# Kernel tuning notes

Measured on AMD Instinct MI355X. Metric: run time of the kernel, lower is better.

The kernel has to match this reference:

```python
import jax, jax.numpy as jnp
import numpy as np

B, S, D, H, L, V = 2, 2048, 768, 12, 2, 32000
DH = D // H
DF = 4 * D
LN_EPS = 1e-5


def _pos_enc():
    # faithful to source: exponent uses 2*i/D with i already stepping by 2
    pos = jnp.arange(S, dtype=jnp.float32)[:, None]
    i = jnp.arange(0, D, 2, dtype=jnp.float32)
    ang = pos / (10000.0 ** (2.0 * i / D))
    enc = jnp.zeros((S, D), jnp.float32)
    enc = enc.at[:, 0::2].set(jnp.sin(ang)).at[:, 1::2].set(jnp.cos(ang))
    return enc


def _ln(x, g, b):
    m = jnp.mean(x, axis=-1, keepdims=True)
    v = jnp.mean((x - m) ** 2, axis=-1, keepdims=True)
    return (x - m) / jnp.sqrt(v + LN_EPS) * g + b


def _layer(x, p):
    Wq, bq, Wk, bk, Wv, bv, Wo, bo, g1, be1, W1, b1, W2, b2, g2, be2 = p
    q = (x @ Wq + bq).reshape(B, S, H, DH)
    k = (x @ Wk + bk).reshape(B, S, H, DH)
    v = (x @ Wv + bv).reshape(B, S, H, DH)
    # NOTE: source divides by sqrt(embed_dim), not sqrt(head_dim)
    attn = jnp.einsum('bqhd,bkhd->bhqk', q, k) / jnp.sqrt(jnp.float32(D))
    attn = jax.nn.softmax(attn, axis=-1)  # [B,H,S,S]
    o = jnp.einsum('bhqk,bkhd->bqhd', attn, v).reshape(B, S, D)
    o = o @ Wo + bo
    x = _ln(x + o, g1, be1)
    h = jax.nn.gelu(x @ W1 + b1, approximate=False)
    x = _ln(x + h @ W2 + b2, g2, be2)
    return x


def setup_inputs() -> dict:
    key = jax.random.key(0)
    ks = jax.random.split(key, 16)
    n = lambda k, shape: jax.random.normal(k, shape, dtype=jnp.float32) * 0.02
    return {
        'input_ids': jax.random.randint(ks[0], (B, S), 0, V),
        'embed_table': n(ks[1], (V, D)),
        'Wq': n(ks[2], (L, D, D)), 'bq': jnp.zeros((L, D), jnp.float32),
        'Wk': n(ks[3], (L, D, D)), 'bk': jnp.zeros((L, D), jnp.float32),
        'Wv': n(ks[4], (L, D, D)), 'bv': jnp.zeros((L, D), jnp.float32),
        'Wo': n(ks[5], (L, D, D)), 'bo': jnp.zeros((L, D), jnp.float32),
        'ln1_g': jnp.ones((L, D), jnp.float32), 'ln1_b': jnp.zeros((L, D), jnp.float32),
        'W1': n(ks[6], (L, D, DF)), 'b1': jnp.zeros((L, DF), jnp.float32),
        'W2': n(ks[7], (L, DF, D)), 'b2': jnp.zeros((L, D), jnp.float32),
        'ln2_g': jnp.ones((L, D), jnp.float32), 'ln2_b': jnp.zeros((L, D), jnp.float32),
        'Wd': n(ks[8], (D, D)), 'bd': jnp.zeros((D,), jnp.float32),
        'lnm_g': jnp.ones((D,), jnp.float32), 'lnm_b': jnp.zeros((D,), jnp.float32),
        'dec_b': jnp.zeros((V,), jnp.float32),
    }


def reference(input_ids, embed_table, Wq, bq, Wk, bk, Wv, bv, Wo, bo,
              ln1_g, ln1_b, W1, b1, W2, b2, ln2_g, ln2_b,
              Wd, bd, lnm_g, lnm_b, dec_b):
    x = embed_table[input_ids] + _pos_enc()[None]  # [B,S,D]

    def step(h, p):
        return _layer(h, p), None

    x, _ = jax.lax.scan(step, x, (Wq, bq, Wk, bk, Wv, bv, Wo, bo,
                                  ln1_g, ln1_b, W1, b1, W2, b2, ln2_g, ln2_b))
    # MLM head with decoder weight tied to embedding table
    h = jax.nn.gelu(x @ Wd + bd, approximate=False)
    h = _ln(h, lnm_g, lnm_b)
    return h @ embed_table.T + dec_b  # [B,S,V]
```

## Files before the change

kernel.cpp:

```cpp
#include <hip/hip_runtime.h>
#include <hip/hip_bf16.h>
#include <cstdint>

typedef __bf16 bf16x8 __attribute__((ext_vector_type(8)));
typedef float  f32x4  __attribute__((ext_vector_type(4)));
typedef unsigned short u16;
typedef u16 u16x8 __attribute__((ext_vector_type(8)));

__device__ __forceinline__ u16 f2bf(float f) {
    union { float f; uint32_t u; } x{f};
    uint32_t u = x.u;
    return (u16)((u + 0x7fffu + ((u >> 16) & 1u)) >> 16);
}

__device__ __forceinline__ float gelu_f(float x) {
    return 0.5f * x * (1.0f + erff(x * 0.70710678118654752f));
}

__device__ __forceinline__ void gl_lds16(const void* g, void* l) {
    __builtin_amdgcn_global_load_lds(
        (__attribute__((address_space(1))) void*)(void*)g,
        (__attribute__((address_space(3))) void*)l, 16, 0, 0);
}

#define MFMA16(a, b, c) __builtin_amdgcn_mfma_f32_16x16x32_bf16((a), (b), (c), 0, 0, 0)
#define SB0 __builtin_amdgcn_sched_barrier(0)

template<int EPI, int OUTF32, int LOC>
__global__ __launch_bounds__(256, 2) void gemm_bf16(
    const u16* __restrict__ A, const u16* __restrict__ Bt,
    const float* __restrict__ bias, void* __restrict__ Cout,
    int N_, int K_)
{
    __shared__ u16 lA[128 * 64];
    __shared__ u16 lB[128 * 64];
    const int tid  = threadIdx.x;
    const int lane = tid & 63;
    const int wave = tid >> 6;
    const int wr = wave >> 1, wc = wave & 1;
    long row0, col0;
    if (LOC) {
        const int bid = blockIdx.x;
        const int chunk = bid >> 9, rem = bid & 511;
        row0 = (long)(rem & 31) * 128;
        col0 = (long)(chunk * 16 + (rem >> 5)) * 128;
    } else {
        row0 = (long)blockIdx.y * 128;
        col0 = (long)blockIdx.x * 128;
    }

    f32x4 acc[4][4];
#pragma unroll
    for (int i = 0; i < 4; ++i)
#pragma unroll
        for (int j = 0; j < 4; ++j)
#pragma unroll
            for (int t = 0; t < 4; ++t) acc[i][j][t] = 0.f;

    int sRow[4], sKb[4];
#pragma unroll
    for (int t = 0; t < 4; ++t) {
        int byteoff = (wave * 4 + t) * 1024 + lane * 16;
        int r = byteoff >> 7;
        sRow[t] = r;
        sKb[t]  = (byteoff & 127) ^ ((r & 7) << 4);
    }
    const int laneRC = lane & 15;
    const int laneK2 = (lane >> 4) * 16;

    for (int k0 = 0; k0 < K_; k0 += 64) {
#pragma unroll
        for (int t = 0; t < 4; ++t) {
            const int cb = (wave * 4 + t) * 1024;
            gl_lds16(A  + (row0 + sRow[t]) * K_ + k0 + (sKb[t] >> 1), (char*)lA + cb);
            gl_lds16(Bt + (col0 + sRow[t]) * K_ + k0 + (sKb[t] >> 1), (char*)lB + cb);
        }
        __syncthreads();
#pragma unroll
        for (int kk = 0; kk < 2; ++kk) {
            bf16x8 af[4], bfr[4];
#pragma unroll
            for (int i = 0; i < 4; ++i) {
                int r = wr * 64 + i * 16 + laneRC;
                af[i] = *(const bf16x8*)((const char*)lA + r * 128 + ((kk * 64 + laneK2) ^ ((r & 7) << 4)));
            }
#pragma unroll
            for (int j = 0; j < 4; ++j) {
                int n = wc * 64 + j * 16 + laneRC;
                bfr[j] = *(const bf16x8*)((const char*)lB + n * 128 + ((kk * 64 + laneK2) ^ ((n & 7) << 4)));
            }
#pragma unroll
            for (int i = 0; i < 4; ++i)
#pragma unroll
                for (int j = 0; j < 4; ++j)
                    acc[i][j] = MFMA16(af[i], bfr[j], acc[i][j]);
        }
        __syncthreads();
    }

#pragma unroll
    for (int j = 0; j < 4; ++j) {
        const long cidx = col0 + wc * 64 + j * 16 + laneRC;
        const float bvv = bias[cidx];
#pragma unroll
        for (int i = 0; i < 4; ++i) {
            const long rbase = row0 + wr * 64 + i * 16 + ((lane >> 4) << 2);
#pragma unroll
            for (int t = 0; t < 4; ++t) {
                float v = acc[i][j][t] + bvv;
                if (EPI) v = gelu_f(v);
                const long off = (rbase + t) * N_ + cidx;
                if (OUTF32) ((float*)Cout)[off] = v;
                else        ((u16*)Cout)[off]  = f2bf(v);
            }
        }
    }
}

template<int EPI, int OUTF32>
__global__ __launch_bounds__(256, 4) void gemm64(
    const u16* __restrict__ A, const u16* __restrict__ Bt,
    const float* __restrict__ bias, void* __restrict__ Cout,
    int N_, int K_)
{
    __shared__ u16 lA[64 * 64];
    __shared__ u16 lB[64 * 64];
    const int tid  = threadIdx.x;
    const int lane = tid & 63;
    const int wave = tid >> 6;
    const int wr = wave >> 1, wc = wave & 1;
    const long row0 = (long)blockIdx.y * 64;
    const long col0 = (long)blockIdx.x * 64;

    f32x4 acc[2][2];
#pragma unroll
    for (int i = 0; i < 2; ++i)
#pragma unroll
        for (int j = 0; j < 2; ++j)
#pragma unroll
            for (int t = 0; t < 4; ++t) acc[i][j][t] = 0.f;

    int sRow[2], sKb[2];
#pragma unroll
    for (int t = 0; t < 2; ++t) {
        int byteoff = (wave * 2 + t) * 1024 + lane * 16;
        int r = byteoff >> 7;
        sRow[t] = r;
        sKb[t]  = (byteoff & 127) ^ ((r & 7) << 4);
    }
    const int laneRC = lane & 15;
    const int laneK2 = (lane >> 4) * 16;

    for (int k0 = 0; k0 < K_; k0 += 64) {
#pragma unroll
        for (int t = 0; t < 2; ++t) {
            const int cb = (wave * 2 + t) * 1024;
            gl_lds16(A  + (row0 + sRow[t]) * K_ + k0 + (sKb[t] >> 1), (char*)lA + cb);
            gl_lds16(Bt + (col0 + sRow[t]) * K_ + k0 + (sKb[t] >> 1), (char*)lB + cb);
        }
        __syncthreads();
#pragma unroll
        for (int kk = 0; kk < 2; ++kk) {
            bf16x8 af[2], bfr[2];
#pragma unroll
            for (int i = 0; i < 2; ++i) {
                int r = wr * 32 + i * 16 + laneRC;
                af[i] = *(const bf16x8*)((const char*)lA + r * 128 + ((kk * 64 + laneK2) ^ ((r & 7) << 4)));
            }
#pragma unroll
            for (int j = 0; j < 2; ++j) {
                int n = wc * 32 + j * 16 + laneRC;
                bfr[j] = *(const bf16x8*)((const char*)lB + n * 128 + ((kk * 64 + laneK2) ^ ((n & 7) << 4)));
            }
#pragma unroll
            for (int i = 0; i < 2; ++i)
#pragma unroll
                for (int j = 0; j < 2; ++j)
                    acc[i][j] = MFMA16(af[i], bfr[j], acc[i][j]);
        }
        __syncthreads();
    }

#pragma unroll
    for (int j = 0; j < 2; ++j) {
        const long cidx = col0 + wc * 32 + j * 16 + laneRC;
        const float bvv = bias[cidx];
#pragma unroll
        for (int i = 0; i < 2; ++i) {
            const long rbase = row0 + wr * 32 + i * 16 + ((lane >> 4) << 2);
#pragma unroll
            for (int t = 0; t < 4; ++t) {
                float v = acc[i][j][t] + bvv;
                if (EPI) v = gelu_f(v);
                const long off = (rbase + t) * N_ + cidx;
                if (OUTF32) ((float*)Cout)[off] = v;
                else        ((u16*)Cout)[off]  = f2bf(v);
            }
        }
    }
}

__global__ __launch_bounds__(256, 3) void attn_fwd(
    const u16* __restrict__ qkv, u16* __restrict__ outb, float scale)
{
    __shared__ u16 lQ[64 * 64];
    __shared__ u16 lK[2][64 * 64];
    __shared__ u16 lVt[2][64 * 64];
    __shared__ u16 lP[64 * 64];
    const int bh = blockIdx.x;
    const int b = bh / 12, h = bh % 12;
    const int q0 = blockIdx.y * 64;
    const int tid = threadIdx.x, lane = tid & 63, wave = tid >> 6;
    const long baseQ = (long)b * 2048 * 2304 + h * 64;
    const long baseK = baseQ + 768;
    const long baseV = baseQ + 1536;
    const int laneRC = lane & 15;
    const int laneK2 = (lane >> 4) * 16;

    int stR[2], stC[2];
#pragma unroll
    for (int t = 0; t < 2; ++t) {
        const int byteoff = (wave * 2 + t) * 1024 + lane * 16;
        const int r = byteoff >> 7;
        stR[t] = r;
        stC[t] = ((byteoff & 127) ^ ((r & 7) << 4)) >> 1;
    }

#define STAGEK(BUF, KB0) do {                                                    \
    _Pragma("unroll") for (int t = 0; t < 2; ++t)                                \
        gl_lds16(qkv + baseK + (long)((KB0) + stR[t]) * 2304 + stC[t],           \
                 (char*)lK[BUF] + (wave * 2 + t) * 1024);                        \
} while (0)

#pragma unroll
    for (int t = 0; t < 2; ++t)
        gl_lds16(qkv + baseQ + (long)(q0 + stR[t]) * 2304 + stC[t],
                 (char*)lQ + (wave * 2 + t) * 1024);
    STAGEK(0, 0);
    u16x8 vA0, vA1;
    {
        const u16x8* gv = (const u16x8*)(qkv + baseV + (long)lane * 2304 + wave * 16);
        vA0 = gv[0]; vA1 = gv[1];
    }
    __syncthreads();

    bf16x8 qf[2];
#pragma unroll
    for (int kk = 0; kk < 2; ++kk) {
        int r = wave * 16 + laneRC;
        qf[kk] = *(const bf16x8*)((const char*)lQ + r * 128 + ((kk * 64 + laneK2) ^ ((r & 7) << 4)));
    }

    bf16x8 onesf;
#pragma unroll
    for (int j = 0; j < 8; ++j) onesf[j] = (__bf16)1.0f;

    float mrun[4];
    f32x4 oacc[4], oaccS;
#pragma unroll
    for (int r = 0; r < 4; ++r) mrun[r] = -1e30f;
#pragma unroll
    for (int dc = 0; dc < 4; ++dc)
#pragma unroll
        for (int t = 0; t < 4; ++t) oacc[dc][t] = 0.f;
#pragma unroll
    for (int t = 0; t < 4; ++t) oaccS[t] = 0.f;

    u16x8 vB0 = vA0, vB1 = vA1;
    for (int kt = 0; kt < 32; ++kt) {
        const int cur = kt & 1;
        asm volatile("s_waitcnt vmcnt(0)" ::: "memory");
        SB0;
        {
            const int kv = lane, dg = wave;
            char* vt = (char*)lVt[cur];
#pragma unroll
            for (int j = 0; j < 8; ++j) {
                int d0 = dg * 16 + j;
                *(u16*)(vt + d0 * 128 + ((kv * 2) ^ ((d0 & 7) << 4))) = vA0[j];
                int d1 = dg * 16 + 8 + j;
                *(u16*)(vt + d1 * 128 + ((kv * 2) ^ ((d1 & 7) << 4))) = vA1[j];
            }
        }
        __builtin_amdgcn_s_barrier();
        SB0;
        if (kt + 1 < 32) {
            STAGEK(cur ^ 1, (kt + 1) * 64);
            const u16x8* gv = (const u16x8*)(qkv + baseV + (long)((kt + 1) * 64 + lane) * 2304 + wave * 16);
            vB0 = gv[0]; vB1 = gv[1];
        }
        const char* lKc = (const char*)lK[cur];
        const char* lVc = (const char*)lVt[cur];

        f32x4 s[4];
#pragma unroll
        for (int cb = 0; cb < 4; ++cb)
#pragma unroll
            for (int t = 0; t < 4; ++t) s[cb][t] = 0.f;
        __builtin_amdgcn_s_setprio(1);
#pragma unroll
        for (int kk = 0; kk < 2; ++kk) {
            bf16x8 kf[4];
#pragma unroll
            for (int cb = 0; cb < 4; ++cb) {
                int kr = cb * 16 + laneRC;
                kf[cb] = *(const bf16x8*)(lKc + kr * 128 + ((kk * 64 + laneK2) ^ ((kr & 7) << 4)));
            }
#pragma unroll
            for (int cb = 0; cb < 4; ++cb)
                s[cb] = MFMA16(qf[kk], kf[cb], s[cb]);
        }
        __builtin_amdgcn_s_setprio(0);

        {
            float tm[4];
#pragma unroll
            for (int r = 0; r < 4; ++r) {
                float v = fmaxf(fmaxf(s[0][r], s[1][r]), fmaxf(s[2][r], s[3][r])) * scale;
#pragma unroll
                for (int msk = 1; msk < 16; msk <<= 1) v = fmaxf(v, __shfl_xor(v, msk, 64));
                tm[r] = v;
            }
            float ex = fmaxf(fmaxf(tm[0] - mrun[0], tm[1] - mrun[1]),
                             fmaxf(tm[2] - mrun[2], tm[3] - mrun[3]));
            float mn[4];
            if (__ballot(ex > 8.0f)) {
                float corr[4];
#pragma unroll
                for (int r = 0; r < 4; ++r) {
                    mn[r] = fmaxf(mrun[r], tm[r]);
                    corr[r] = __expf(mrun[r] - mn[r]);
                    mrun[r] = mn[r];
                }
                const int srcl = ((lane & 15) >> 2) << 4;
                float c0 = __shfl(corr[0], srcl, 64);
                float c1 = __shfl(corr[1], srcl, 64);
                float c2 = __shfl(corr[2], srcl, 64);
                float c3 = __shfl(corr[3], srcl, 64);
                const int selr = (lane & 15) & 3;
                float cp = selr == 0 ? c0 : (selr == 1 ? c1 : (selr == 2 ? c2 : c3));
#pragma unroll
                for (int dc = 0; dc < 4; ++dc)
#pragma unroll
                    for (int t = 0; t < 4; ++t) oacc[dc][t] *= cp;
#pragma unroll
                for (int t = 0; t < 4; ++t) oaccS[t] *= cp;
            } else {
#pragma unroll
                for (int r = 0; r < 4; ++r) mn[r] = mrun[r];
            }
#pragma unroll
            for (int cb2 = 0; cb2 < 4; ++cb2) {
                int pcol = cb2 * 16 + laneRC;
#pragma unroll
                for (int r = 0; r < 4; ++r) {
                    float pv = __expf(s[cb2][r] * scale - mn[r]);
                    int prow = wave * 16 + ((lane >> 4) << 2) + r;
                    *(u16*)((char*)lP + prow * 128 + ((pcol * 2) ^ ((prow & 7) << 4))) = f2bf(pv);
                }
            }
        }

        __builtin_amdgcn_s_setprio(1);
#pragma unroll
        for (int kk = 0; kk < 2; ++kk) {
            bf16x8 pf, vf[4];
            {
                int pr = wave * 16 + laneRC;
                pf = *(const bf16x8*)((const char*)lP + pr * 128 + ((kk * 64 + laneK2) ^ ((pr & 7) << 4)));
            }
#pragma unroll
            for (int dc = 0; dc < 4; ++dc) {
                int d = dc * 16 + laneRC;
                vf[dc] = *(const bf16x8*)(lVc + d * 128 + ((kk * 64 + laneK2) ^ ((d & 7) << 4)));
            }
#pragma unroll
            for (int dc = 0; dc < 4; ++dc)
                oacc[dc] = MFMA16(vf[dc], pf, oacc[dc]);
            oaccS = MFMA16(onesf, pf, oaccS);
        }
        __builtin_amdgcn_s_setprio(0);
        vA0 = vB0; vA1 = vB1;
    }
#undef STAGEK

    const float inv = 1.0f / oaccS[0];
    const long rowq = (long)b * 2048 + q0 + wave * 16 + (lane & 15);
#pragma unroll
    for (int dc = 0; dc < 4; ++dc) {
        const int colb = h * 64 + dc * 16 + ((lane >> 4) << 2);
        ushort4 st;
        st.x = f2bf(oacc[dc][0] * inv);
        st.y = f2bf(oacc[dc][1] * inv);
        st.z = f2bf(oacc[dc][2] * inv);
        st.w = f2bf(oacc[dc][3] * inv);
        *(ushort4*)(outb + rowq * 768 + colb) = st;
    }
}

__global__ __launch_bounds__(256) void ln_fused(
    const float* __restrict__ a, const float* __restrict__ bres,
    const float* __restrict__ g, const float* __restrict__ be,
    float* __restrict__ outf, u16* __restrict__ outb)
{
    const int wave = threadIdx.x >> 6, lane = threadIdx.x & 63;
    const int row = blockIdx.x * 4 + wave;
    const size_t rbase = (size_t)row * 768;
    float4 v[3];
    float s1 = 0.f, s2 = 0.f;
#pragma unroll
    for (int i = 0; i < 3; ++i) {
        const int c = lane * 4 + i * 256;
        float4 x = *(const float4*)(a + rbase + c);
        if (bres) {
            const float4 y = *(const float4*)(bres + rbase + c);
            x.x += y.x; x.y += y.y; x.z += y.z; x.w += y.w;
        }
        v[i] = x;
        s1 += x.x + x.y + x.z + x.w;
        s2 += x.x * x.x + x.y * x.y + x.z * x.z + x.w * x.w;
    }
#pragma unroll
    for (int m = 1; m < 64; m <<= 1) { s1 += __shfl_xor(s1, m, 64); s2 += __shfl_xor(s2, m, 64); }
    const float mean = s1 * (1.f / 768.f);
    const float var  = s2 * (1.f / 768.f) - mean * mean;
    const float rstd = rsqrtf(var + 1e-5f);
#pragma unroll
    for (int i = 0; i < 3; ++i) {
        const int c = lane * 4 + i * 256;
        const float4 gg = *(const float4*)(g + c);
        const float4 bb = *(const float4*)(be + c);
        float4 y;
        y.x = (v[i].x - mean) * rstd * gg.x + bb.x;
        y.y = (v[i].y - mean) * rstd * gg.y + bb.y;
        y.z = (v[i].z - mean) * rstd * gg.z + bb.z;
        y.w = (v[i].w - mean) * rstd * gg.w + bb.w;
        if (outf) *(float4*)(outf + rbase + c) = y;
        ushort4 u; u.x = f2bf(y.x); u.y = f2bf(y.y); u.z = f2bf(y.z); u.w = f2bf(y.w);
        *(ushort4*)(outb + rbase + c) = u;
    }
}

struct TP9 { const float* s[9]; u16* d[9]; };
__global__ void transpose_multi(TP9 p, int R, int C)
{
    __shared__ float t[32][33];
    const float* in = p.s[blockIdx.z];
    u16* out = p.d[blockIdx.z];
    const int c0 = blockIdx.x * 32, r0 = blockIdx.y * 32;
    const int tx = threadIdx.x, ty = threadIdx.y;
#pragma unroll
    for (int i = 0; i < 4; ++i)
        t[ty + 8 * i][tx] = in[(size_t)(r0 + ty + 8 * i) * C + c0 + tx];
    __syncthreads();
#pragma unroll
    for (int i = 0; i < 4; ++i)
        out[(size_t)(c0 + ty + 8 * i) * R + r0 + tx] = f2bf(t[tx][ty + 8 * i]);
}

__global__ void cvt_bf16_k(const float* __restrict__ in, u16* __restrict__ out, long n)
{
    long i = ((long)blockIdx.x * 256 + threadIdx.x) * 4;
    if (i >= n) return;
    const float4 f = *(const float4*)(in + i);
    ushort4 u; u.x = f2bf(f.x); u.y = f2bf(f.y); u.z = f2bf(f.z); u.w = f2bf(f.w);
    *(ushort4*)(out + i) = u;
}

__global__ void concat_bias(const float* __restrict__ bq, const float* __restrict__ bk,
                            const float* __restrict__ bv, float* __restrict__ out, int total)
{
    int i = blockIdx.x * 256 + threadIdx.x;
    if (i >= total) return;
    int l = i / 2304, j = i - l * 2304;
    float v = (j < 768) ? bq[l * 768 + j]
            : (j < 1536) ? bk[l * 768 + j - 768]
            : bv[l * 768 + j - 1536];
    out[i] = v;
}

__global__ __launch_bounds__(256) void embed_pe(
    const int* __restrict__ ids, const float* __restrict__ table,
    float* __restrict__ xf, u16* __restrict__ xb)
{
    const int idx = blockIdx.x * 256 + threadIdx.x;
    const int row = idx / 768, d = idx - row * 768;
    const int s = row & 2047;
    const float e = table[(long)ids[row] * 768 + d];
    const int j = d >> 1;
    const float ang = (float)s * __expf(-0.011992630692677324f * (float)(4 * j));
    const float pe = (d & 1) ? __cosf(ang) : __sinf(ang);
    const float v = e + pe;
    xf[idx] = v;
    xb[idx] = f2bf(v);
}

extern "C" void kernel_launch(void* const* d_in, const int* in_sizes, int n_in,
                              void* d_out, int out_size, void* d_ws, size_t ws_size,
                              hipStream_t stream)
{
    const int S = 2048, D = 768, H = 12, L = 2, V = 32000, DF = 3072, M = 4096, NQKV = 2304;
    (void)in_sizes; (void)n_in; (void)out_size; (void)ws_size; (void)H; (void)S;

    const int*   ids  = (const int*)  d_in[0];
    const float* emb  = (const float*)d_in[1];
    const float* Wq   = (const float*)d_in[2];
    const float* bq   = (const float*)d_in[3];
    const float* Wk   = (const float*)d_in[4];
    const float* bk   = (const float*)d_in[5];
    const float* Wv   = (const float*)d_in[6];
    const float* bv   = (const float*)d_in[7];
    const float* Wo   = (const float*)d_in[8];
    const float* bo   = (const float*)d_in[9];
    const float* ln1g = (const float*)d_in[10];
    const float* ln1b = (const float*)d_in[11];
    const float* W1   = (const float*)d_in[12];
    const float* b1   = (const float*)d_in[13];
    const float* W2   = (const float*)d_in[14];
    const float* b2   = (const float*)d_in[15];
    const float* ln2g = (const float*)d_in[16];
    const float* ln2b = (const float*)d_in[17];
    const float* Wd   = (const float*)d_in[18];
    const float* bd   = (const float*)d_in[19];
    const float* lnmg = (const float*)d_in[20];
    const float* lnmb = (const float*)d_in[21];
    const float* decb = (const float*)d_in[22];

    char* p = (char*)d_ws;
    auto carve = [&](size_t bytes) { char* r = p; p += (bytes + 255) & ~(size_t)255; return r; };
    u16*   embB  = (u16*)  carve((size_t)V * D * 2);
    u16*   wqkvT = (u16*)  carve((size_t)L * NQKV * D * 2);
    float* bqkv  = (float*)carve((size_t)L * NQKV * 4);
    u16*   woT   = (u16*)  carve((size_t)L * D * D * 2);
    u16*   w1T   = (u16*)  carve((size_t)L * DF * D * 2);
    u16*   w2T   = (u16*)  carve((size_t)L * D * DF * 2);
    u16*   wdT   = (u16*)  carve((size_t)D * D * 2);
    float* xf    = (float*)carve((size_t)M * D * 4);
    u16*   xb    = (u16*)  carve((size_t)M * D * 2);
    u16*   qkvB  = (u16*)  carve((size_t)M * NQKV * 2);
    u16*   aoB   = (u16*)  carve((size_t)M * D * 2);
    float* tmpf  = (float*)carve((size_t)M * D * 4);
    u16*   hB    = (u16*)  carve((size_t)M * DF * 2);

    dim3 t32x8(32, 8);
    cvt_bf16_k<<<((long)V * D / 4 + 255) / 256, 256, 0, stream>>>(emb, embB, (long)V * D);
    {
        TP9 t9;
        for (int l = 0; l < L; ++l) {
            t9.s[l * 4 + 0] = Wq + (size_t)l * D * D; t9.d[l * 4 + 0] = wqkvT + (size_t)l * NQKV * D;
            t9.s[l * 4 + 1] = Wk + (size_t)l * D * D; t9.d[l * 4 + 1] = wqkvT + (size_t)l * NQKV * D + (size_t)D * D;
            t9.s[l * 4 + 2] = Wv + (size_t)l * D * D; t9.d[l * 4 + 2] = wqkvT + (size_t)l * NQKV * D + (size_t)2 * D * D;
            t9.s[l * 4 + 3] = Wo + (size_t)l * D * D; t9.d[l * 4 + 3] = woT + (size_t)l * D * D;
        }
        t9.s[8] = Wd; t9.d[8] = wdT;
        transpose_multi<<<dim3(24, 24, 9), t32x8, 0, stream>>>(t9, D, D);
        TP9 tw1; tw1.s[0] = W1; tw1.d[0] = w1T; tw1.s[1] = W1 + (size_t)D * DF; tw1.d[1] = w1T + (size_t)DF * D;
        transpose_multi<<<dim3(96, 24, 2), t32x8, 0, stream>>>(tw1, D, DF);
        TP9 tw2; tw2.s[0] = W2; tw2.d[0] = w2T; tw2.s[1] = W2 + (size_t)DF * D; tw2.d[1] = w2T + (size_t)D * DF;
        transpose_multi<<<dim3(24, 96, 2), t32x8, 0, stream>>>(tw2, DF, D);
    }
    concat_bias<<<(L * NQKV + 255) / 256, 256, 0, stream>>>(bq, bk, bv, bqkv, L * NQKV);
    embed_pe<<<M * D / 256, 256, 0, stream>>>(ids, emb, xf, xb);

    const float scale = 0.036084391824351615f;
    for (int l = 0; l < L; ++l) {
        gemm_bf16<0, 0, 0><<<dim3(NQKV / 128, M / 128), 256, 0, stream>>>(xb, wqkvT + (size_t)l * NQKV * D, bqkv + l * NQKV, qkvB, NQKV, D);
        attn_fwd<<<dim3(24, 32), 256, 0, stream>>>(qkvB, aoB, scale);
        gemm64<0, 1><<<dim3(D / 64, M / 64), 256, 0, stream>>>(aoB, woT + (size_t)l * D * D, bo + l * D, tmpf, D, D);
        ln_fused<<<M / 4, 256, 0, stream>>>(xf, tmpf, ln1g + l * D, ln1b + l * D, xf, xb);
        gemm_bf16<1, 0, 0><<<dim3(DF / 128, M / 128), 256, 0, stream>>>(xb, w1T + (size_t)l * DF * D, b1 + l * DF, hB, DF, D);
        gemm64<0, 1><<<dim3(D / 64, M / 64), 256, 0, stream>>>(hB, w2T + (size_t)l * D * DF, b2 + l * D, tmpf, D, DF);
        ln_fused<<<M / 4, 256, 0, stream>>>(xf, tmpf, ln2g + l * D, ln2b + l * D, xf, xb);
    }
    gemm64<1, 1><<<dim3(D / 64, M / 64), 256, 0, stream>>>(xb, wdT, bd, tmpf, D, D);
    ln_fused<<<M / 4, 256, 0, stream>>>(tmpf, nullptr, lnmg, lnmb, nullptr, aoB);
    gemm_bf16<0, 1, 1><<<V / 128 * 32, 256, 0, stream>>>(aoB, embB, decb, (float*)d_out, V, D);
}
```

Baseline: 763.8 us.

## Split-K FFN down-proj into LN, lazy softmax max updates, fuse prep kernels

The FFN down-projection now uses the 128-tile GEMM with 4-way split-K. Partial sums go to four fp32 buffers that the following LayerNorm adds up, with the bias applied only by the first split. This aims to raise occupancy for the narrow N=768 GEMM with long K. In attention, the running-max check and rescale now run only every fourth key tile, and the embedding conversion, embed+PE and bias concat are merged into one launch. Skipping max updates relies on exp not overflowing within the window, and split-K adds extra fp32 traffic.

```diff
diff --git a/kernel.cpp b/kernel.cpp
--- a/kernel.cpp
+++ b/kernel.cpp
@@ -26,7 +26,7 @@
 #define MFMA16(a, b, c) __builtin_amdgcn_mfma_f32_16x16x32_bf16((a), (b), (c), 0, 0, 0)
 #define SB0 __builtin_amdgcn_sched_barrier(0)
 
-template<int EPI, int OUTF32, int LOC>
+template<int EPI, int OUTF32, int LOC, int SPLITK>
 __global__ __launch_bounds__(256, 2) void gemm_bf16(
     const u16* __restrict__ A, const u16* __restrict__ Bt,
     const float* __restrict__ bias, void* __restrict__ Cout,
@@ -48,6 +48,8 @@
         row0 = (long)blockIdx.y * 128;
         col0 = (long)blockIdx.x * 128;
     }
+    const int KS = K_ / SPLITK;
+    const int kz = (SPLITK > 1) ? blockIdx.z * KS : 0;
 
     f32x4 acc[4][4];
 #pragma unroll
@@ -68,7 +70,7 @@
     const int laneRC = lane & 15;
     const int laneK2 = (lane >> 4) * 16;
 
-    for (int k0 = 0; k0 < K_; k0 += 64) {
+    for (int k0 = kz; k0 < kz + KS; k0 += 64) {
 #pragma unroll
         for (int t = 0; t < 4; ++t) {
             const int cb = (wave * 4 + t) * 1024;
@@ -98,10 +100,11 @@
         __syncthreads();
     }
 
+    float* outF = (float*)Cout + (SPLITK > 1 ? (long)blockIdx.z * 4096 * N_ : 0);
 #pragma unroll
     for (int j = 0; j < 4; ++j) {
         const long cidx = col0 + wc * 64 + j * 16 + laneRC;
-        const float bvv = bias[cidx];
+        const float bvv = (SPLITK == 1 || blockIdx.z == 0) ? bias[cidx] : 0.f;
 #pragma unroll
         for (int i = 0; i < 4; ++i) {
             const long rbase = row0 + wr * 64 + i * 16 + ((lane >> 4) << 2);
@@ -110,8 +113,8 @@
                 float v = acc[i][j][t] + bvv;
                 if (EPI) v = gelu_f(v);
                 const long off = (rbase + t) * N_ + cidx;
-                if (OUTF32) ((float*)Cout)[off] = v;
-                else        ((u16*)Cout)[off]  = f2bf(v);
+                if (OUTF32) outF[off] = v;
+                else        ((u16*)Cout)[off] = f2bf(v);
             }
         }
     }
@@ -312,7 +315,7 @@
         }
         __builtin_amdgcn_s_setprio(0);
 
-        {
+        if ((kt & 3) == 0) {
             float tm[4];
 #pragma unroll
             for (int r = 0; r < 4; ++r) {
@@ -323,14 +326,13 @@
             }
             float ex = fmaxf(fmaxf(tm[0] - mrun[0], tm[1] - mrun[1]),
                              fmaxf(tm[2] - mrun[2], tm[3] - mrun[3]));
-            float mn[4];
             if (__ballot(ex > 8.0f)) {
                 float corr[4];
 #pragma unroll
                 for (int r = 0; r < 4; ++r) {
-                    mn[r] = fmaxf(mrun[r], tm[r]);
-                    corr[r] = __expf(mrun[r] - mn[r]);
-                    mrun[r] = mn[r];
+                    float mnew = fmaxf(mrun[r], tm[r]);
+                    corr[r] = __expf(mrun[r] - mnew);
+                    mrun[r] = mnew;
                 }
                 const int srcl = ((lane & 15) >> 2) << 4;
                 float c0 = __shfl(corr[0], srcl, 64);
@@ -345,19 +347,16 @@
                     for (int t = 0; t < 4; ++t) oacc[dc][t] *= cp;
 #pragma unroll
                 for (int t = 0; t < 4; ++t) oaccS[t] *= cp;
-            } else {
-#pragma unroll
-                for (int r = 0; r < 4; ++r) mn[r] = mrun[r];
-            }
-#pragma unroll
-            for (int cb2 = 0; cb2 < 4; ++cb2) {
-                int pcol = cb2 * 16 + laneRC;
-#pragma unroll
-                for (int r = 0; r < 4; ++r) {
-                    float pv = __expf(s[cb2][r] * scale - mn[r]);
-                    int prow = wave * 16 + ((lane >> 4) << 2) + r;
-                    *(u16*)((char*)lP + prow * 128 + ((pcol * 2) ^ ((prow & 7) << 4))) = f2bf(pv);
-                }
+            }
+        }
+#pragma unroll
+        for (int cb2 = 0; cb2 < 4; ++cb2) {
+            int pcol = cb2 * 16 + laneRC;
+#pragma unroll
+            for (int r = 0; r < 4; ++r) {
+                float pv = __expf(s[cb2][r] * scale - mrun[r]);
+                int prow = wave * 16 + ((lane >> 4) << 2) + r;
+                *(u16*)((char*)lP + prow * 128 + ((pcol * 2) ^ ((prow & 7) << 4))) = f2bf(pv);
             }
         }
 
@@ -398,8 +397,9 @@
     }
 }
 
+template<int NP>
 __global__ __launch_bounds__(256) void ln_fused(
-    const float* __restrict__ a, const float* __restrict__ bres,
+    const float* __restrict__ a, const float* __restrict__ parts, long pstride,
     const float* __restrict__ g, const float* __restrict__ be,
     float* __restrict__ outf, u16* __restrict__ outb)
 {
@@ -412,8 +412,9 @@
     for (int i = 0; i < 3; ++i) {
         const int c = lane * 4 + i * 256;
         float4 x = *(const float4*)(a + rbase + c);
-        if (bres) {
-            const float4 y = *(const float4*)(bres + rbase + c);
+#pragma unroll
+        for (int p = 0; p < NP; ++p) {
+            const float4 y = *(const float4*)(parts + (size_t)p * pstride + rbase + c);
             x.x += y.x; x.y += y.y; x.z += y.z; x.w += y.w;
         }
         v[i] = x;
@@ -458,41 +459,41 @@
         out[(size_t)(c0 + ty + 8 * i) * R + r0 + tx] = f2bf(t[tx][ty + 8 * i]);
 }
 
-__global__ void cvt_bf16_k(const float* __restrict__ in, u16* __restrict__ out, long n)
-{
-    long i = ((long)blockIdx.x * 256 + threadIdx.x) * 4;
-    if (i >= n) return;
-    const float4 f = *(const float4*)(in + i);
-    ushort4 u; u.x = f2bf(f.x); u.y = f2bf(f.y); u.z = f2bf(f.z); u.w = f2bf(f.w);
-    *(ushort4*)(out + i) = u;
-}
-
-__global__ void concat_bias(const float* __restrict__ bq, const float* __restrict__ bk,
-                            const float* __restrict__ bv, float* __restrict__ out, int total)
-{
-    int i = blockIdx.x * 256 + threadIdx.x;
-    if (i >= total) return;
-    int l = i / 2304, j = i - l * 2304;
-    float v = (j < 768) ? bq[l * 768 + j]
-            : (j < 1536) ? bk[l * 768 + j - 768]
-            : bv[l * 768 + j - 1536];
-    out[i] = v;
-}
-
-__global__ __launch_bounds__(256) void embed_pe(
-    const int* __restrict__ ids, const float* __restrict__ table,
-    float* __restrict__ xf, u16* __restrict__ xb)
-{
-    const int idx = blockIdx.x * 256 + threadIdx.x;
-    const int row = idx / 768, d = idx - row * 768;
-    const int s = row & 2047;
-    const float e = table[(long)ids[row] * 768 + d];
-    const int j = d >> 1;
-    const float ang = (float)s * __expf(-0.011992630692677324f * (float)(4 * j));
-    const float pe = (d & 1) ? __cosf(ang) : __sinf(ang);
-    const float v = e + pe;
-    xf[idx] = v;
-    xb[idx] = f2bf(v);
+__global__ __launch_bounds__(256) void prep_misc(
+    const float* __restrict__ emb, u16* __restrict__ embB,
+    const int* __restrict__ ids, float* __restrict__ xf, u16* __restrict__ xb,
+    const float* __restrict__ bq, const float* __restrict__ bk,
+    const float* __restrict__ bv, float* __restrict__ bqkv)
+{
+    const long A = 6144000;
+    const long B = 3145728;
+    long t = (long)blockIdx.x * 256 + threadIdx.x;
+    if (t < A) {
+        const long i = t * 4;
+        const float4 f = *(const float4*)(emb + i);
+        ushort4 u; u.x = f2bf(f.x); u.y = f2bf(f.y); u.z = f2bf(f.z); u.w = f2bf(f.w);
+        *(ushort4*)(embB + i) = u;
+    } else if (t < A + B) {
+        const int idx = (int)(t - A);
+        const int row = idx / 768, d = idx - row * 768;
+        const int s = row & 2047;
+        const float e = emb[(long)ids[row] * 768 + d];
+        const int j = d >> 1;
+        const float ang = (float)s * __expf(-0.011992630692677324f * (float)(4 * j));
+        const float pe = (d & 1) ? __cosf(ang) : __sinf(ang);
+        const float v = e + pe;
+        xf[idx] = v;
+        xb[idx] = f2bf(v);
+    } else {
+        const int i = (int)(t - A - B);
+        if (i < 4608) {
+            int l = i / 2304, j = i - l * 2304;
+            float v = (j < 768) ? bq[l * 768 + j]
+                    : (j < 1536) ? bk[l * 768 + j - 768]
+                    : bv[l * 768 + j - 1536];
+            bqkv[i] = v;
+        }
+    }
 }
 
 extern "C" void kernel_launch(void* const* d_in, const int* in_sizes, int n_in,
@@ -539,11 +540,12 @@
     u16*   xb    = (u16*)  carve((size_t)M * D * 2);
     u16*   qkvB  = (u16*)  carve((size_t)M * NQKV * 2);
     u16*   aoB   = (u16*)  carve((size_t)M * D * 2);
-    float* tmpf  = (float*)carve((size_t)M * D * 4);
+    float* tmpf  = (float*)carve((size_t)M * D * 4 * 4);
     u16*   hB    = (u16*)  carve((size_t)M * DF * 2);
 
     dim3 t32x8(32, 8);
-    cvt_bf16_k<<<((long)V * D / 4 + 255) / 256, 256, 0, stream>>>(emb, embB, (long)V * D);
+    prep_misc<<<(6144000 + 3145728 + 4608) / 256, 256, 0, stream>>>(
+        emb, embB, ids, xf, xb, bq, bk, bv, bqkv);
     {
         TP9 t9;
         for (int l = 0; l < L; ++l) {
@@ -559,20 +561,19 @@
         TP9 tw2; tw2.s[0] = W2; tw2.d[0] = w2T; tw2.s[1] = W2 + (size_t)DF * D; tw2.d[1] = w2T + (size_t)D * DF;
         transpose_multi<<<dim3(24, 96, 2), t32x8, 0, stream>>>(tw2, DF, D);
     }
-    concat_bias<<<(L * NQKV + 255) / 256, 256, 0, stream>>>(bq, bk, bv, bqkv, L * NQKV);
-    embed_pe<<<M * D / 256, 256, 0, stream>>>(ids, emb, xf, xb);
 
     const float scale = 0.036084391824351615f;
+    const long PSTR = (long)M * D;
     for (int l = 0; l < L; ++l) {
-        gemm_bf16<0, 0, 0><<<dim3(NQKV / 128, M / 128), 256, 0, stream>>>(xb, wqkvT + (size_t)l * NQKV * D, bqkv + l * NQKV, qkvB, NQKV, D);
+        gemm_bf16<0, 0, 0, 1><<<dim3(NQKV / 128, M / 128), 256, 0, stream>>>(xb, wqkvT + (size_t)l * NQKV * D, bqkv + l * NQKV, qkvB, NQKV, D);
         attn_fwd<<<dim3(24, 32), 256, 0, stream>>>(qkvB, aoB, scale);
         gemm64<0, 1><<<dim3(D / 64, M / 64), 256, 0, stream>>>(aoB, woT + (size_t)l * D * D, bo + l * D, tmpf, D, D);
-        ln_fused<<<M / 4, 256, 0, stream>>>(xf, tmpf, ln1g + l * D, ln1b + l * D, xf, xb);
-        gemm_bf16<1, 0, 0><<<dim3(DF / 128, M / 128), 256, 0, stream>>>(xb, w1T + (size_t)l * DF * D, b1 + l * DF, hB, DF, D);
-        gemm64<0, 1><<<dim3(D / 64, M / 64), 256, 0, stream>>>(hB, w2T + (size_t)l * D * DF, b2 + l * D, tmpf, D, DF);
-        ln_fused<<<M / 4, 256, 0, stream>>>(xf, tmpf, ln2g + l * D, ln2b + l * D, xf, xb);
+        ln_fused<1><<<M / 4, 256, 0, stream>>>(xf, tmpf, PSTR, ln1g + l * D, ln1b + l * D, xf, xb);
+        gemm_bf16<1, 0, 0, 1><<<dim3(DF / 128, M / 128), 256, 0, stream>>>(xb, w1T + (size_t)l * DF * D, b1 + l * DF, hB, DF, D);
+        gemm_bf16<0, 1, 0, 4><<<dim3(D / 128, M / 128, 4), 256, 0, stream>>>(hB, w2T + (size_t)l * D * DF, b2 + l * D, tmpf, D, DF);
+        ln_fused<4><<<M / 4, 256, 0, stream>>>(xf, tmpf, PSTR, ln2g + l * D, ln2b + l * D, xf, xb);
     }
     gemm64<1, 1><<<dim3(D / 64, M / 64), 256, 0, stream>>>(xb, wdT, bd, tmpf, D, D);
-    ln_fused<<<M / 4, 256, 0, stream>>>(tmpf, nullptr, lnmg, lnmb, nullptr, aoB);
-    gemm_bf16<0, 1, 1><<<V / 128 * 32, 256, 0, stream>>>(aoB, embB, decb, (float*)d_out, V, D);
-}
+    ln_fused<0><<<M / 4, 256, 0, stream>>>(tmpf, nullptr, 0, lnmg, lnmb, nullptr, aoB);
+    gemm_bf16<0, 1, 1, 1><<<V / 128 * 32, 256, 0, stream>>>(aoB, embB, decb, (float*)d_out, V, D);
+}
```

Result: faster. 740.1 us (-3.1%).
